# Kernel tuning notes

Measured on AMD Instinct MI355X. Metric: run time of the kernel, lower is better.

Reference implementation:

```python
import jax, jax.numpy as jnp
import numpy as np

B, TQ, TK, D, NA = 8, 512, 2048, 1024, 512
H, HD = 16, 64          # n_head, head_dim (D = H*HD)
NE, HID = 4, 32         # n_experts, expert hidden_dim
EPS = 1e-6


def _rmsnorm(x, w):
    return x * jax.lax.rsqrt(jnp.mean(x * x, axis=-1, keepdims=True) + EPS) * w


def setup_inputs() -> dict:
    key = jax.random.key(0)
    ks = jax.random.split(key, 20)
    r = lambda i, shp: jax.random.normal(ks[i], shp, dtype=jnp.float32) * 0.02
    return {
        'q': jax.random.normal(ks[0], (B, TQ, D), dtype=jnp.float32),
        'kv': jax.random.normal(ks[1], (B, TK, D), dtype=jnp.float32),
        'qn_w': jnp.ones((D,), jnp.float32),
        'kva_w': jnp.ones((D,), jnp.float32),
        'kvi_w': jnp.ones((D,), jnp.float32),
        'dn_w': jnp.ones((D,), jnp.float32),
        'fn_w': jnp.ones((D,), jnp.float32),
        'Wq': r(2, (D, D)), 'bq': jnp.zeros((D,), jnp.float32),
        'Wk': r(3, (D, D)), 'bk': jnp.zeros((D,), jnp.float32),
        'Wv': r(4, (D, D)), 'bv': jnp.zeros((D,), jnp.float32),
        'Wo': r(5, (D, D)), 'bo': jnp.zeros((D,), jnp.float32),
        'active_bias': r(6, (D,)),
        'inactive_bias': r(7, (D,)),
        'log_temp': jnp.array(0.0, jnp.float32),
        'gate_attn': jnp.array(0.3, jnp.float32),
        'gate_ffn': jnp.array(0.7, jnp.float32),
        'Wr': r(8, (D, NE)), 'br': jnp.zeros((NE,), jnp.float32),
        'W1': r(9, (NE, D, 2 * HID)), 'b1': jnp.zeros((NE, 2 * HID), jnp.float32),
        'W2': r(10, (NE, HID, D)), 'b2': jnp.zeros((NE, D), jnp.float32),
        'kv_mask': jnp.ones((B, TK), bool),
        'n_actives': NA,
    }


def _forward(q, kv, qn_w, kva_w, kvi_w, dn_w, fn_w,
             Wq, bq, Wk, bk, Wv, bv, Wo, bo,
             active_bias, inactive_bias, log_temp, gate_attn, gate_ffn,
             Wr, br, W1, b1, W2, b2, kv_mask, n_actives):
    Na = int(n_actives)
    Tk = kv.shape[1]
    Ni = Tk - Na
    b, tq, d = q.shape

    # split-normed kv, with active/inactive learned biases injected pre-KV-proj
    kv_a = _rmsnorm(kv[:, :Na], kva_w) + active_bias
    kv_i = _rmsnorm(kv[:, Na:], kvi_w) + inactive_bias
    kv_b = jnp.concatenate([kv_a, kv_i], axis=1)

    qn = _rmsnorm(q, qn_w)
    qp = (qn @ Wq + bq).reshape(b, tq, H, HD).transpose(0, 2, 1, 3)  # (B,H,Tq,hd)
    k = (kv_b @ Wk + bk).reshape(b, Tk, H, HD).transpose(0, 2, 1, 3)
    v = (kv_b @ Wv + bv).reshape(b, Tk, H, HD).transpose(0, 2, 1, 3)

    # torch: q *= 1/sqrt(hd), then SDPA(q/temp, ...) applies another 1/sqrt(hd)
    temp = jnp.clip(jnp.exp(log_temp), 0.1, 10.0)
    scale = 1.0 / (HD * temp)

    def attn(kk, vv):
        logits = jnp.einsum('bhqd,bhkd->bhqk', qp, kk) * scale
        return jnp.einsum('bhqk,bhkd->bhqd', jax.nn.softmax(logits, axis=-1), vv)

    out = attn(k[:, :, :Na], v[:, :, :Na]) / np.sqrt(max(Na, 1)) \
        - attn(k[:, :, Na:], v[:, :, Na:]) / np.sqrt(max(Ni, 1))
    out = out.transpose(0, 2, 1, 3).reshape(b, tq, d)
    delta = _rmsnorm(out @ Wo + bo, dn_w)
    q_new = q + jax.nn.sigmoid(gate_attn) * delta

    # dense soft MoE over normed kv, with query-similarity logit bias
    x = _rmsnorm(kv, fn_w)
    logits = x @ Wr + br                                   # (B,Tk,NE)
    q_vec = jnp.mean(q_new, axis=1, keepdims=True)         # (B,1,D)
    sim = jnp.einsum('bqd,btd->bt', q_vec, x)              # (B,Tk)
    probs = jax.nn.softmax(logits + sim[..., None], axis=-1)

    h = jnp.einsum('btd,edh->bteh', x, W1) + b1            # (B,Tk,NE,2*HID)
    xp, g = h[..., :HID], h[..., HID:]
    act = xp * (g * jax.nn.sigmoid(g))                     # SwiGLU
    eo = jnp.einsum('bteh,ehd->bted', act, W2) + b2        # (B,Tk,NE,D)
    moe_out = jnp.einsum('bte,bted->btd', probs, eo)

    kv_new = kv + jax.nn.sigmoid(gate_ffn) * moe_out
    return q_new, kv_new


def reference(q, kv, qn_w, kva_w, kvi_w, dn_w, fn_w,
              Wq, bq, Wk, bk, Wv, bv, Wo, bo,
              active_bias, inactive_bias, log_temp, gate_attn, gate_ffn,
              Wr, br, W1, b1, W2, b2, kv_mask, n_actives):
    return _forward(q, kv, qn_w, kva_w, kvi_w, dn_w, fn_w,
                    Wq, bq, Wk, bk, Wv, bv, Wo, bo,
                    active_bias, inactive_bias, log_temp, gate_attn, gate_ffn,
                    Wr, br, W1, b1, W2, b2, kv_mask, n_actives)
```

## Files before the change

kernel.cpp:

```cpp
#include <hip/hip_runtime.h>
#include <hip/hip_bf16.h>
#include <stdint.h>


#define B_   8
#define TQ_  512
#define TK_  2048
#define D_   1024
#define H_   16
#define HD_  64
#define NE_  4
#define HID_ 32
#define EPSF 1e-6f
#define LOG2E 1.44269504f

typedef __bf16 bf16_t;
typedef __bf16 bf16x8 __attribute__((ext_vector_type(8)));
typedef __bf16 bf16x4 __attribute__((ext_vector_type(4)));
typedef float  f32x4  __attribute__((ext_vector_type(4)));

typedef __attribute__((address_space(1))) void gvoid_t;
typedef __attribute__((address_space(3))) void lvoid_t;

__device__ __forceinline__ void gld_lds16(const void* g, void* l) {
  __builtin_amdgcn_global_load_lds((gvoid_t*)g, (lvoid_t*)l, 16, 0, 0);
}

__global__ void transpose_conv_kernel(const float* __restrict__ in, bf16_t* __restrict__ out,
                                      int R, int C, int in_bstride,
                                      int out_rstride, int ob_row, int ob_col) {
  __shared__ float tile[32][33];
  const int bz = blockIdx.z;
  const int rb = blockIdx.y * 32, cb = blockIdx.x * 32;
  const int txi = threadIdx.x, tyi = threadIdx.y;
  const float* inp = in + (size_t)bz * in_bstride;
#pragma unroll
  for (int i = 0; i < 32; i += 8) {
    const int r = rb + tyi + i, c = cb + txi;
    if (r < R && c < C) tile[tyi + i][txi] = inp[(size_t)r * C + c];
  }
  __syncthreads();
#pragma unroll
  for (int i = 0; i < 32; i += 8) {
    const int orow = cb + tyi + i;
    const int ocol = rb + txi;
    if (orow < C && ocol < R)
      out[(size_t)(orow + bz * ob_row) * out_rstride + bz * ob_col + ocol] =
          (bf16_t)tile[txi][tyi + i];
  }
}

__device__ __forceinline__ float block_rsum(float v, float* red) {
  v += __shfl_xor(v, 1);  v += __shfl_xor(v, 2);  v += __shfl_xor(v, 4);
  v += __shfl_xor(v, 8);  v += __shfl_xor(v, 16); v += __shfl_xor(v, 32);
  const int tid = threadIdx.x;
  if ((tid & 63) == 0) red[tid >> 6] = v;
  __syncthreads();
  return red[0] + red[1] + red[2] + red[3];
}

__global__ __launch_bounds__(256)
void rms_kv_kernel(const float* __restrict__ kv, const float* __restrict__ kva_w,
                   const float* __restrict__ kvi_w, const float* __restrict__ fn_w,
                   const float* __restrict__ ab, const float* __restrict__ ib,
                   const int* __restrict__ n_act, const float* __restrict__ Wr,
                   const float* __restrict__ br,
                   bf16_t* __restrict__ kvb, bf16_t* __restrict__ xn,
                   float* __restrict__ probs) {
  __shared__ float red[4];
  __shared__ f32x4 pred[4];
  const int row = blockIdx.x;
  const int t = row & (TK_ - 1);
  const int tid = threadIdx.x;
  const float* src = kv + (size_t)row * D_;
  f32x4 v = ((const f32x4*)src)[tid];
  float ss = v[0]*v[0] + v[1]*v[1] + v[2]*v[2] + v[3]*v[3];
  ss = block_rsum(ss, red);
  const float rs = rsqrtf(ss * (1.0f / D_) + EPSF);
  const int Na = n_act[0];
  const float* wsel = (t < Na) ? kva_w : kvi_w;
  const float* bsel = (t < Na) ? ab : ib;
  const int d = tid * 4;
  f32x4 wv = *(const f32x4*)(wsel + d);
  f32x4 bv = *(const f32x4*)(bsel + d);
  f32x4 fv = *(const f32x4*)(fn_w + d);
  bf16x4 o0, o1;
  f32x4 p4 = {};
#pragma unroll
  for (int c = 0; c < 4; ++c) {
    const float xv = v[c] * rs;
    const float xf = xv * fv[c];
    o0[c] = (bf16_t)(xv * wv[c] + bv[c]);
    o1[c] = (bf16_t)xf;
    const f32x4 w4 = *(const f32x4*)&Wr[(d + c) * 4];
    p4 += w4 * xf;
  }
  *(bf16x4*)&kvb[(size_t)row * D_ + d] = o0;
  *(bf16x4*)&xn [(size_t)row * D_ + d] = o1;
#pragma unroll
  for (int m = 1; m <= 32; m <<= 1) {
    p4[0] += __shfl_xor(p4[0], m); p4[1] += __shfl_xor(p4[1], m);
    p4[2] += __shfl_xor(p4[2], m); p4[3] += __shfl_xor(p4[3], m);
  }
  if ((tid & 63) == 0) pred[tid >> 6] = p4;
  __syncthreads();
  if (tid == 0) {
    f32x4 s = pred[0] + pred[1] + pred[2] + pred[3];
    s[0] += br[0]; s[1] += br[1]; s[2] += br[2]; s[3] += br[3];
    const float mx = fmaxf(fmaxf(s[0], s[1]), fmaxf(s[2], s[3]));
    const float e0 = __expf(s[0] - mx), e1 = __expf(s[1] - mx);
    const float e2 = __expf(s[2] - mx), e3 = __expf(s[3] - mx);
    const float inv = 1.0f / (e0 + e1 + e2 + e3);
    f32x4 pr = { e0 * inv, e1 * inv, e2 * inv, e3 * inv };
    *(f32x4*)&probs[row * 4] = pr;
  }
}

__global__ __launch_bounds__(256)
void rms_q_kernel(const float* __restrict__ q, const float* __restrict__ qn_w,
                  bf16_t* __restrict__ qn) {
  __shared__ float red[4];
  const int row = blockIdx.x;
  const int tid = threadIdx.x;
  const float* src = q + (size_t)row * D_;
  f32x4 v = ((const f32x4*)src)[tid];
  float ss = v[0]*v[0] + v[1]*v[1] + v[2]*v[2] + v[3]*v[3];
  ss = block_rsum(ss, red);
  const float rs = rsqrtf(ss * (1.0f / D_) + EPSF);
  const int d = tid * 4;
  f32x4 wv = *(const f32x4*)(qn_w + d);
  bf16x4 o0;
#pragma unroll
  for (int c = 0; c < 4; ++c) o0[c] = (bf16_t)(v[c] * rs * wv[c]);
  *(bf16x4*)&qn[(size_t)row * D_ + d] = o0;
}

__device__ __forceinline__ void gemm_loop_db(const bf16_t* __restrict__ ga,
                                             const bf16_t* __restrict__ gb,
                                             bf16_t* As, bf16_t* Bs, int K,
                                             size_t rstep, int ar, int br2,
                                             int tid, f32x4 acc[4][4]) {
  gld_lds16(ga,         &As[tid * 8]);
  gld_lds16(ga + rstep, &As[2048 + tid * 8]);
  gld_lds16(gb,         &Bs[tid * 8]);
  gld_lds16(gb + rstep, &Bs[2048 + tid * 8]);
  int buf = 0;
  for (int k0 = 0; k0 < K; k0 += 32) {
    __syncthreads();
    if (k0 + 32 < K) {
      const int nb = buf ^ 1;
      gld_lds16(ga + k0 + 32,         &As[nb * 4096 + tid * 8]);
      gld_lds16(ga + k0 + 32 + rstep, &As[nb * 4096 + 2048 + tid * 8]);
      gld_lds16(gb + k0 + 32,         &Bs[nb * 4096 + tid * 8]);
      gld_lds16(gb + k0 + 32 + rstep, &Bs[nb * 4096 + 2048 + tid * 8]);
    }
    bf16x8 af[4], bfr[4];
#pragma unroll
    for (int i = 0; i < 4; ++i) af[i]  = *(const bf16x8*)&As[buf * 4096 + ar  + i * 512];
#pragma unroll
    for (int j = 0; j < 4; ++j) bfr[j] = *(const bf16x8*)&Bs[buf * 4096 + br2 + j * 512];
#pragma unroll
    for (int i = 0; i < 4; ++i)
#pragma unroll
      for (int j = 0; j < 4; ++j)
        acc[i][j] = __builtin_amdgcn_mfma_f32_16x16x32_bf16(af[i], bfr[j], acc[i][j], 0, 0, 0);
    buf ^= 1;
  }
}

__device__ __forceinline__ int xcd_swz(int bx, int gx) {
  if ((gx & 7) == 0) { const int cpx = gx >> 3; return (bx & 7) * cpx + (bx >> 3); }
  return bx;
}

template<int HAS_BIAS>
__global__ __launch_bounds__(256)
void gemm_tn(const bf16_t* __restrict__ A, const bf16_t* __restrict__ Wt,
             const float* __restrict__ bias, bf16_t* __restrict__ C,
             int M, int N, int K) {
  __shared__ alignas(16) bf16_t As[2 * 128 * 32];
  __shared__ alignas(16) bf16_t Bs[2 * 128 * 32];
  const int tid = threadIdx.x;
  const int lane = tid & 63;
  const int w = tid >> 6;
  const int wr = w >> 1, wc = w & 1;
  const int m0 = xcd_swz(blockIdx.x, gridDim.x) * 128;
  const int n0 = blockIdx.y * 128;

  f32x4 acc[4][4] = {};
  const int eidx = tid * 8;
  const int srow = eidx >> 5;
  const int scol = eidx & 31;
  const bf16_t* ga = A  + (size_t)(m0 + srow) * K + scol;
  const bf16_t* gb = Wt + (size_t)(n0 + srow) * K + scol;
  const int kb = (lane >> 4) * 8;
  const int ar  = (wr * 64 + (lane & 15)) * 32 + kb;
  const int br2 = (wc * 64 + (lane & 15)) * 32 + kb;

  gemm_loop_db(ga, gb, As, Bs, K, (size_t)64 * K, ar, br2, tid, acc);

  const int row0 = m0 + wr * 64 + ((lane >> 4) << 2);
  const int col0 = n0 + wc * 64 + (lane & 15);
#pragma unroll
  for (int j = 0; j < 4; ++j) {
    const int cc = col0 + j * 16;
    const float bv = HAS_BIAS ? bias[cc] : 0.0f;
#pragma unroll
    for (int i = 0; i < 4; ++i) {
      const int rr = row0 + i * 16;
#pragma unroll
      for (int r = 0; r < 4; ++r)
        C[(size_t)(rr + r) * N + cc] = (bf16_t)(acc[i][j][r] + bv);
    }
  }
}

__global__ __launch_bounds__(256)
void gemm_vt(const bf16_t* __restrict__ A, const bf16_t* __restrict__ Wt0,
             const float* __restrict__ bias, bf16_t* __restrict__ C0) {
  __shared__ alignas(16) bf16_t As[2 * 128 * 32];
  __shared__ alignas(16) bf16_t Bs[2 * 128 * 32];
  const int K = D_, N = TK_;
  const bf16_t* Wt = Wt0 + (size_t)blockIdx.z * TK_ * D_;
  bf16_t* C = C0 + (size_t)blockIdx.z * D_ * TK_;
  const int tid = threadIdx.x;
  const int lane = tid & 63;
  const int w = tid >> 6;
  const int wr = w >> 1, wc = w & 1;
  const int m0 = blockIdx.x * 128;
  const int n0 = blockIdx.y * 128;

  f32x4 acc[4][4] = {};
  const int eidx = tid * 8;
  const int srow = eidx >> 5;
  const int scol = eidx & 31;
  const bf16_t* ga = A  + (size_t)(m0 + srow) * K + scol;
  const bf16_t* gb = Wt + (size_t)(n0 + srow) * K + scol;
  const int kb = (lane >> 4) * 8;
  const int ar  = (wr * 64 + (lane & 15)) * 32 + kb;
  const int br2 = (wc * 64 + (lane & 15)) * 32 + kb;

  gemm_loop_db(ga, gb, As, Bs, K, (size_t)64 * K, ar, br2, tid, acc);

  const int row0 = m0 + wr * 64 + ((lane >> 4) << 2);
  const int col0 = n0 + wc * 64 + (lane & 15);
#pragma unroll
  for (int i = 0; i < 4; ++i) {
    const int rr = row0 + i * 16;
#pragma unroll
    for (int r = 0; r < 4; ++r) {
      const float bv = bias[rr + r];
#pragma unroll
      for (int j = 0; j < 4; ++j)
        C[(size_t)(rr + r) * N + col0 + j * 16] = (bf16_t)(acc[i][j][r] + bv);
    }
  }
}

__global__ __launch_bounds__(256)
void gemm_h_act(const bf16_t* __restrict__ A, const bf16_t* __restrict__ Wt,
                const float* __restrict__ bias, const float* __restrict__ probs,
                bf16_t* __restrict__ a2) {
  __shared__ alignas(16) bf16_t As[2 * 128 * 32];
  __shared__ alignas(16) bf16_t Bs[2 * 128 * 32];
  const int K = D_;
  const int tid = threadIdx.x;
  const int lane = tid & 63;
  const int w = tid >> 6;
  const int wr = w >> 1, wc = w & 1;
  const int m0 = xcd_swz(blockIdx.x, gridDim.x) * 128;
  const int n0 = blockIdx.y * 128;

  f32x4 acc[4][4] = {};
  const int eidx = tid * 8;
  const int srow = eidx >> 5;
  const int scol = eidx & 31;
  const bf16_t* ga = A  + (size_t)(m0 + srow) * K + scol;
  const bf16_t* gb = Wt + (size_t)(n0 + srow) * K + scol;
  const int kb = (lane >> 4) * 8;
  const int ar  = (wr * 64 + (lane & 15)) * 32 + kb;
  const int br2 = (wc * 64 + (lane & 15)) * 32 + kb;

  gemm_loop_db(ga, gb, As, Bs, K, (size_t)64 * K, ar, br2, tid, acc);

  const int row0 = m0 + wr * 64 + ((lane >> 4) << 2);
  const int hbase = n0 + wc * 64 + (lane & 15);
  const int e = hbase >> 6;
#pragma unroll
  for (int j = 0; j < 2; ++j) {
    const int ch = hbase + j * 16;
    const float bx = bias[ch], bg = bias[ch + 32];
    const int ac = (ch & 63) + e * 32;
#pragma unroll
    for (int i = 0; i < 4; ++i) {
      const int rr = row0 + i * 16;
#pragma unroll
      for (int r = 0; r < 4; ++r) {
        const float xp = acc[i][j][r] + bx;
        const float g  = acc[i][j + 2][r] + bg;
        const float sg = 1.0f / (1.0f + __expf(-g));
        const float pr = probs[(size_t)(rr + r) * 4 + e];
        a2[(size_t)(rr + r) * 128 + ac] = (bf16_t)(pr * xp * g * sg);
      }
    }
  }
}

__global__ __launch_bounds__(256)
void gemm_moe_kvnew(const bf16_t* __restrict__ A, const bf16_t* __restrict__ Wt,
                    const float* __restrict__ kv, const float* __restrict__ probs,
                    const float* __restrict__ b2, const float* __restrict__ gate_ffn,
                    float* __restrict__ out) {
  __shared__ alignas(16) bf16_t As[2 * 128 * 32];
  __shared__ alignas(16) bf16_t Bs[2 * 128 * 32];
  const int K = 128, N = D_;
  const int tid = threadIdx.x;
  const int lane = tid & 63;
  const int w = tid >> 6;
  const int wr = w >> 1, wc = w & 1;
  const int m0 = xcd_swz(blockIdx.x, gridDim.x) * 128;
  const int n0 = blockIdx.y * 128;

  f32x4 acc[4][4] = {};
  const int eidx = tid * 8;
  const int srow = eidx >> 5;
  const int scol = eidx & 31;
  const bf16_t* ga = A  + (size_t)(m0 + srow) * K + scol;
  const bf16_t* gb = Wt + (size_t)(n0 + srow) * K + scol;
  const int kb = (lane >> 4) * 8;
  const int ar  = (wr * 64 + (lane & 15)) * 32 + kb;
  const int br2 = (wc * 64 + (lane & 15)) * 32 + kb;

  gemm_loop_db(ga, gb, As, Bs, K, (size_t)64 * K, ar, br2, tid, acc);

  const float sgf = 1.0f / (1.0f + __expf(-gate_ffn[0]));
  const int row0 = m0 + wr * 64 + ((lane >> 4) << 2);
  const int col0 = n0 + wc * 64 + (lane & 15);
#pragma unroll
  for (int j = 0; j < 4; ++j) {
    const int cc = col0 + j * 16;
    const f32x4 b2v = { b2[0 * D_ + cc], b2[1 * D_ + cc], b2[2 * D_ + cc], b2[3 * D_ + cc] };
#pragma unroll
    for (int i = 0; i < 4; ++i) {
      const int rr = row0 + i * 16;
#pragma unroll
      for (int r = 0; r < 4; ++r) {
        const f32x4 pr = *(const f32x4*)&probs[(size_t)(rr + r) * 4];
        const float bsum = pr[0]*b2v[0] + pr[1]*b2v[1] + pr[2]*b2v[2] + pr[3]*b2v[3];
        out[(size_t)(rr + r) * N + cc] =
            kv[(size_t)(rr + r) * N + cc] + sgf * (acc[i][j][r] + bsum);
      }
    }
  }
}

__global__ __launch_bounds__(512, 2)
void attn_mfma_kernel(const bf16_t* __restrict__ qp, const bf16_t* __restrict__ kb,
                      const bf16_t* __restrict__ vt, bf16_t* __restrict__ attno,
                      const float* __restrict__ log_temp, const int* __restrict__ n_act) {
  __shared__ alignas(16) bf16_t Ks[2][64 * 64];
  __shared__ alignas(16) bf16_t Vs[2][64 * 64];
  __shared__ alignas(16) bf16_t Ps[8][16 * 64];

  const int dd = blockIdx.x;
  const int xcd = dd & 7, within = dd >> 3;
  const int qt = within & 3, slot0 = within >> 2;
  const int bh = slot0 * 8 + xcd;
  const int b = bh >> 4, h = bh & 15;

  const int tid = threadIdx.x;
  const int lane = tid & 63;
  const int w = tid >> 6;
  const int lane15 = lane & 15, lgrp = lane >> 4, l7 = lane & 7;
  const int Na = n_act[0];
  float temp = __expf(log_temp[0]);
  temp = fminf(fmaxf(temp, 0.1f), 10.0f);
  const float lsc = LOG2E / (64.0f * temp);
  const int q0 = qt * 128;

  const bf16_t* qsrc = qp + (size_t)(b * TQ_ + q0 + w * 16 + lane15) * D_ + h * 64 + lgrp * 8;
  bf16x8 qf0 = *(const bf16x8*)qsrc;
  bf16x8 qf1 = *(const bf16x8*)(qsrc + 32);
#pragma unroll
  for (int j = 0; j < 8; ++j) {
    qf0[j] = (bf16_t)((float)qf0[j] * lsc);
    qf1[j] = (bf16_t)((float)qf1[j] * lsc);
  }

  const int srow = tid >> 3;
  const int schunk = (tid & 7) ^ (srow & 7);
  const bf16_t* ksrc = kb + (size_t)(b * TK_ + srow) * D_ + h * 64 + schunk * 8;
  const bf16_t* vsrc = vt + ((size_t)(b * 16 + h) * 64 + srow) * TK_ + schunk * 8;

  f32x4 o[4] = {};
  f32x4 outa[4] = {};
  float lacc = 0.f;

  const float inv_sa = rsqrtf((float)(Na > 1 ? Na : 1));
  const int Ni = TK_ - Na;
  const float inv_si = rsqrtf((float)(Ni > 1 ? Ni : 1));

  gld_lds16(ksrc, &Ks[0][tid * 8]);
  gld_lds16(vsrc, &Vs[0][tid * 8]);

  for (int t = 0; t < TK_ / 64; ++t) {
    const int cur = t & 1;
    __syncthreads();
    if (t + 1 < TK_ / 64) {
      const int nb = cur ^ 1;
      gld_lds16(ksrc + (size_t)(t + 1) * 64 * D_, &Ks[nb][tid * 8]);
      gld_lds16(vsrc + (size_t)(t + 1) * 64,      &Vs[nb][tid * 8]);
    }

    f32x4 sacc[4];
#pragma unroll
    for (int cf = 0; cf < 4; ++cf) {
      const int krow = (cf * 16 + lane15) * 64;
      const bf16x8 kf0 = *(const bf16x8*)&Ks[cur][krow + ((lgrp ^ l7) << 3)];
      const bf16x8 kf1 = *(const bf16x8*)&Ks[cur][krow + (((lgrp + 4) ^ l7) << 3)];
      f32x4 s = {};
      s = __builtin_amdgcn_mfma_f32_16x16x32_bf16(kf0, qf0, s, 0, 0, 0);
      s = __builtin_amdgcn_mfma_f32_16x16x32_bf16(kf1, qf1, s, 0, 0, 0);
      sacc[cf] = s;
    }

#pragma unroll
    for (int cf = 0; cf < 4; ++cf) {
      f32x4 p;
#pragma unroll
      for (int r = 0; r < 4; ++r) p[r] = exp2f(sacc[cf][r]);
      lacc += (p[0] + p[1]) + (p[2] + p[3]);
      bf16x4 pv4;
#pragma unroll
      for (int r = 0; r < 4; ++r) pv4[r] = (bf16_t)p[r];
      const int c = cf * 2 + (lgrp >> 1);
      *(bf16x4*)&Ps[w][lane15 * 64 + ((c ^ l7) << 3) + (lgrp & 1) * 4] = pv4;
    }

    {
      const int prow = lane15 * 64;
      const bf16x8 pa0 = *(const bf16x8*)&Ps[w][prow + ((lgrp ^ l7) << 3)];
      const bf16x8 pa1 = *(const bf16x8*)&Ps[w][prow + (((lgrp + 4) ^ l7) << 3)];
#pragma unroll
      for (int df = 0; df < 4; ++df) {
        const int vrow = (df * 16 + lane15) * 64;
        const bf16x8 vf0 = *(const bf16x8*)&Vs[cur][vrow + ((lgrp ^ l7) << 3)];
        const bf16x8 vf1 = *(const bf16x8*)&Vs[cur][vrow + (((lgrp + 4) ^ l7) << 3)];
        o[df] = __builtin_amdgcn_mfma_f32_16x16x32_bf16(pa0, vf0, o[df], 0, 0, 0);
        o[df] = __builtin_amdgcn_mfma_f32_16x16x32_bf16(pa1, vf1, o[df], 0, 0, 0);
      }
    }

    const bool endA = ((t + 1) * 64 == Na);
    const bool endI = (t == TK_ / 64 - 1);
    if (endA || endI) {
      float l = lacc;
      l += __shfl_xor(l, 16);
      l += __shfl_xor(l, 32);
      const float ssc = endA ? inv_sa : -inv_si;
      f32x4 iv;
#pragma unroll
      for (int r = 0; r < 4; ++r) iv[r] = ssc / __shfl(l, lgrp * 4 + r);
#pragma unroll
      for (int df = 0; df < 4; ++df) { outa[df] += o[df] * iv; o[df] = (f32x4){}; }
      lacc = 0.f;
    }
  }

#pragma unroll
  for (int df = 0; df < 4; ++df)
#pragma unroll
    for (int r = 0; r < 4; ++r)
      attno[(size_t)(b * TQ_ + q0 + w * 16 + lgrp * 4 + r) * D_ + h * 64 + df * 16 + lane15] =
          (bf16_t)outa[df][r];
}

__global__ __launch_bounds__(256)
void delta_qnew_kernel(const bf16_t* __restrict__ proj, const float* __restrict__ dn_w,
                       const float* __restrict__ q, const float* __restrict__ gate_attn,
                       float* __restrict__ qnew) {
  __shared__ float red[4];
  const int row = blockIdx.x;
  const int tid = threadIdx.x;
  bf16x4 pv = *(const bf16x4*)(proj + (size_t)row * D_ + tid * 4);
  f32x4 v;
#pragma unroll
  for (int c = 0; c < 4; ++c) v[c] = (float)pv[c];
  float ss = v[0]*v[0] + v[1]*v[1] + v[2]*v[2] + v[3]*v[3];
  ss = block_rsum(ss, red);
  const float rs = rsqrtf(ss * (1.0f / D_) + EPSF);
  const float sga = 1.0f / (1.0f + __expf(-gate_attn[0]));
  const int d = tid * 4;
  f32x4 wv = *(const f32x4*)(dn_w + d);
  f32x4 qv = *(const f32x4*)(q + (size_t)row * D_ + d);
  f32x4 out;
#pragma unroll
  for (int c = 0; c < 4; ++c) out[c] = qv[c] + sga * (v[c] * rs * wv[c]);
  *(f32x4*)&qnew[(size_t)row * D_ + d] = out;
}

extern "C" void kernel_launch(void* const* d_in, const int* in_sizes, int n_in,
                              void* d_out, int out_size, void* d_ws, size_t ws_size,
                              hipStream_t stream) {
  const float* q           = (const float*)d_in[0];
  const float* kv          = (const float*)d_in[1];
  const float* qn_w        = (const float*)d_in[2];
  const float* kva_w       = (const float*)d_in[3];
  const float* kvi_w       = (const float*)d_in[4];
  const float* dn_w        = (const float*)d_in[5];
  const float* fn_w        = (const float*)d_in[6];
  const float* Wq          = (const float*)d_in[7];
  const float* bq          = (const float*)d_in[8];
  const float* Wk          = (const float*)d_in[9];
  const float* bk          = (const float*)d_in[10];
  const float* Wv          = (const float*)d_in[11];
  const float* bv          = (const float*)d_in[12];
  const float* Wo          = (const float*)d_in[13];
  const float* bo          = (const float*)d_in[14];
  const float* active_bias = (const float*)d_in[15];
  const float* inactive_b  = (const float*)d_in[16];
  const float* log_temp    = (const float*)d_in[17];
  const float* gate_attn   = (const float*)d_in[18];
  const float* gate_ffn    = (const float*)d_in[19];
  const float* Wr          = (const float*)d_in[20];
  const float* br          = (const float*)d_in[21];
  const float* W1          = (const float*)d_in[22];
  const float* b1          = (const float*)d_in[23];
  const float* W2          = (const float*)d_in[24];
  const float* b2          = (const float*)d_in[25];
  const int*   n_act       = (const int*)d_in[27];

  char* ws = (char*)d_ws;
  size_t off = 0;
  auto alloc = [&](size_t bytes) -> char* {
    char* p = ws + off;
    off = (off + bytes + 255) & ~(size_t)255;
    return p;
  };

  bf16_t* wqT  = (bf16_t*)alloc((size_t)D_ * D_ * 2);
  bf16_t* wkT  = (bf16_t*)alloc((size_t)D_ * D_ * 2);
  bf16_t* wvT  = (bf16_t*)alloc((size_t)D_ * D_ * 2);
  bf16_t* woT  = (bf16_t*)alloc((size_t)D_ * D_ * 2);
  bf16_t* w1T  = (bf16_t*)alloc((size_t)256 * D_ * 2);
  bf16_t* w2T  = (bf16_t*)alloc((size_t)D_ * 128 * 2);
  bf16_t* kvb  = (bf16_t*)alloc((size_t)B_ * TK_ * D_ * 2);
  bf16_t* xn   = (bf16_t*)alloc((size_t)B_ * TK_ * D_ * 2);
  bf16_t* qn   = (bf16_t*)alloc((size_t)B_ * TQ_ * D_ * 2);
  bf16_t* qp   = (bf16_t*)alloc((size_t)B_ * TQ_ * D_ * 2);
  bf16_t* kbuf = (bf16_t*)alloc((size_t)B_ * TK_ * D_ * 2);
  bf16_t* vt   = (bf16_t*)alloc((size_t)B_ * D_ * TK_ * 2);
  float*  probs = (float*)alloc((size_t)B_ * TK_ * NE_ * 4);
  bf16_t* attno = qn;
  bf16_t* proj  = qp;
  bf16_t* a2buf = kbuf;
  (void)ws_size; (void)in_sizes; (void)n_in; (void)out_size;

  float* q_new_out  = (float*)d_out;
  float* kv_new_out = (float*)d_out + (size_t)B_ * TQ_ * D_;

  dim3 tb(32, 8);
  transpose_conv_kernel<<<dim3(32, 32, 1), tb, 0, stream>>>(Wq, wqT, D_, D_, 0, D_, 0, 0);
  transpose_conv_kernel<<<dim3(32, 32, 1), tb, 0, stream>>>(Wk, wkT, D_, D_, 0, D_, 0, 0);
  transpose_conv_kernel<<<dim3(32, 32, 1), tb, 0, stream>>>(Wv, wvT, D_, D_, 0, D_, 0, 0);
  transpose_conv_kernel<<<dim3(32, 32, 1), tb, 0, stream>>>(Wo, woT, D_, D_, 0, D_, 0, 0);
  transpose_conv_kernel<<<dim3(2, 32, 4), tb, 0, stream>>>(W1, w1T, D_, 64, D_ * 64, D_, 64, 0);
  transpose_conv_kernel<<<dim3(32, 1, 4), tb, 0, stream>>>(W2, w2T, 32, D_, 32 * D_, 128, 0, 32);

  rms_kv_kernel<<<B_ * TK_, 256, 0, stream>>>(kv, kva_w, kvi_w, fn_w, active_bias,
                                              inactive_b, n_act, Wr, br, kvb, xn, probs);
  rms_q_kernel<<<B_ * TQ_, 256, 0, stream>>>(q, qn_w, qn);

  gemm_tn<1><<<dim3(B_ * TQ_ / 128, D_ / 128), 256, 0, stream>>>(qn, wqT, bq, qp, B_ * TQ_, D_, D_);
  gemm_tn<1><<<dim3(B_ * TK_ / 128, D_ / 128), 256, 0, stream>>>(kvb, wkT, bk, kbuf, B_ * TK_, D_, D_);
  gemm_vt<<<dim3(D_ / 128, TK_ / 128, B_), 256, 0, stream>>>(wvT, kvb, bv, vt);

  attn_mfma_kernel<<<B_ * H_ * (TQ_ / 128), 512, 0, stream>>>(qp, kbuf, vt, attno, log_temp, n_act);

  gemm_tn<1><<<dim3(B_ * TQ_ / 128, D_ / 128), 256, 0, stream>>>(attno, woT, bo, proj, B_ * TQ_, D_, D_);
  delta_qnew_kernel<<<B_ * TQ_, 256, 0, stream>>>(proj, dn_w, q, gate_attn, q_new_out);

  gemm_h_act<<<dim3(B_ * TK_ / 128, 2), 256, 0, stream>>>(xn, w1T, b1, probs, a2buf);
  gemm_moe_kvnew<<<dim3(B_ * TK_ / 128, D_ / 128), 256, 0, stream>>>(a2buf, w2T, kv, probs, b2,
                                                                     gate_ffn, kv_new_out);
}
```

Measured before the change: 357.3 us.

## Restructure attention to 32 rows per wave, add 64-row GEMMs, batch transposes

The attention kernel drops from 512 to 256 threads per block. Each wave now handles 32 query rows, so every K/V fragment read from LDS feeds two MFMA streams, and s_setprio hints are added around the MFMA sections. New 64-row-tile GEMM variants replace the Q-projection, output-projection and MoE-hidden GEMMs to raise block counts on the smaller problems. The four weight transposes are merged into one launch. In exchange the attention kernel uses more registers per wave and runs with fewer waves per block.

```diff
diff --git a/kernel.cpp b/kernel.cpp
--- a/kernel.cpp
+++ b/kernel.cpp
@@ -24,6 +24,24 @@
 
 __device__ __forceinline__ void gld_lds16(const void* g, void* l) {
   __builtin_amdgcn_global_load_lds((gvoid_t*)g, (lvoid_t*)l, 16, 0, 0);
+}
+
+struct TP4 { const float* in[4]; bf16_t* out[4]; };
+
+__global__ void transpose_conv4_kernel(TP4 p) {
+  __shared__ float tile[32][33];
+  const int bz = blockIdx.z;
+  const float* in = p.in[bz];
+  bf16_t* out = p.out[bz];
+  const int rb = blockIdx.y * 32, cb = blockIdx.x * 32;
+  const int txi = threadIdx.x, tyi = threadIdx.y;
+#pragma unroll
+  for (int i = 0; i < 32; i += 8)
+    tile[tyi + i][txi] = in[(size_t)(rb + tyi + i) * D_ + cb + txi];
+  __syncthreads();
+#pragma unroll
+  for (int i = 0; i < 32; i += 8)
+    out[(size_t)(cb + tyi + i) * D_ + rb + txi] = (bf16_t)tile[txi][tyi + i];
 }
 
 __global__ void transpose_conv_kernel(const float* __restrict__ in, bf16_t* __restrict__ out,
@@ -133,6 +151,11 @@
 #pragma unroll
   for (int c = 0; c < 4; ++c) o0[c] = (bf16_t)(v[c] * rs * wv[c]);
   *(bf16x4*)&qn[(size_t)row * D_ + d] = o0;
+}
+
+__device__ __forceinline__ int xcd_swz(int bx, int gx) {
+  if ((gx & 7) == 0) { const int cpx = gx >> 3; return (bx & 7) * cpx + (bx >> 3); }
+  return bx;
 }
 
 __device__ __forceinline__ void gemm_loop_db(const bf16_t* __restrict__ ga,
@@ -168,9 +191,35 @@
   }
 }
 
-__device__ __forceinline__ int xcd_swz(int bx, int gx) {
-  if ((gx & 7) == 0) { const int cpx = gx >> 3; return (bx & 7) * cpx + (bx >> 3); }
-  return bx;
+__device__ __forceinline__ void gemm64_loop_db(const bf16_t* __restrict__ ga,
+                                               const bf16_t* __restrict__ gb,
+                                               bf16_t* As, bf16_t* Bs, int K,
+                                               size_t rstep, int ar, int br2,
+                                               int tid, f32x4 acc[2][4]) {
+  gld_lds16(ga,         &As[tid * 8]);
+  gld_lds16(gb,         &Bs[tid * 8]);
+  gld_lds16(gb + rstep, &Bs[2048 + tid * 8]);
+  int buf = 0;
+  for (int k0 = 0; k0 < K; k0 += 32) {
+    __syncthreads();
+    if (k0 + 32 < K) {
+      const int nb = buf ^ 1;
+      gld_lds16(ga + k0 + 32,         &As[nb * 2048 + tid * 8]);
+      gld_lds16(gb + k0 + 32,         &Bs[nb * 4096 + tid * 8]);
+      gld_lds16(gb + k0 + 32 + rstep, &Bs[nb * 4096 + 2048 + tid * 8]);
+    }
+    bf16x8 af[2], bfr[4];
+#pragma unroll
+    for (int i = 0; i < 2; ++i) af[i]  = *(const bf16x8*)&As[buf * 2048 + ar  + i * 512];
+#pragma unroll
+    for (int j = 0; j < 4; ++j) bfr[j] = *(const bf16x8*)&Bs[buf * 4096 + br2 + j * 512];
+#pragma unroll
+    for (int i = 0; i < 2; ++i)
+#pragma unroll
+      for (int j = 0; j < 4; ++j)
+        acc[i][j] = __builtin_amdgcn_mfma_f32_16x16x32_bf16(af[i], bfr[j], acc[i][j], 0, 0, 0);
+    buf ^= 1;
+  }
 }
 
 template<int HAS_BIAS>
@@ -188,14 +237,11 @@
   const int n0 = blockIdx.y * 128;
 
   f32x4 acc[4][4] = {};
-  const int eidx = tid * 8;
-  const int srow = eidx >> 5;
-  const int scol = eidx & 31;
-  const bf16_t* ga = A  + (size_t)(m0 + srow) * K + scol;
-  const bf16_t* gb = Wt + (size_t)(n0 + srow) * K + scol;
+  const bf16_t* ga = A  + (size_t)(m0 + (tid >> 2)) * K + (tid & 3) * 8;
+  const bf16_t* gb = Wt + (size_t)(n0 + (tid >> 2)) * K + (tid & 3) * 8;
   const int kb = (lane >> 4) * 8;
-  const int ar  = (wr * 64 + (lane & 15)) * 32 + kb;
-  const int br2 = (wc * 64 + (lane & 15)) * 32 + kb;
+  const int ar  = ((wr * 64 + (lane & 15)) << 5) + kb;
+  const int br2 = ((wc * 64 + (lane & 15)) << 5) + kb;
 
   gemm_loop_db(ga, gb, As, Bs, K, (size_t)64 * K, ar, br2, tid, acc);
 
@@ -207,6 +253,45 @@
     const float bv = HAS_BIAS ? bias[cc] : 0.0f;
 #pragma unroll
     for (int i = 0; i < 4; ++i) {
+      const int rr = row0 + i * 16;
+#pragma unroll
+      for (int r = 0; r < 4; ++r)
+        C[(size_t)(rr + r) * N + cc] = (bf16_t)(acc[i][j][r] + bv);
+    }
+  }
+}
+
+template<int HAS_BIAS>
+__global__ __launch_bounds__(256)
+void gemm64_tn(const bf16_t* __restrict__ A, const bf16_t* __restrict__ Wt,
+               const float* __restrict__ bias, bf16_t* __restrict__ C,
+               int M, int N, int K) {
+  __shared__ alignas(16) bf16_t As[2 * 64 * 32];
+  __shared__ alignas(16) bf16_t Bs[2 * 128 * 32];
+  const int tid = threadIdx.x;
+  const int lane = tid & 63;
+  const int w = tid >> 6;
+  const int wr = w >> 1, wc = w & 1;
+  const int m0 = xcd_swz(blockIdx.x, gridDim.x) * 64;
+  const int n0 = blockIdx.y * 128;
+
+  f32x4 acc[2][4] = {};
+  const bf16_t* ga = A  + (size_t)(m0 + (tid >> 2)) * K + (tid & 3) * 8;
+  const bf16_t* gb = Wt + (size_t)(n0 + (tid >> 2)) * K + (tid & 3) * 8;
+  const int kb = (lane >> 4) * 8;
+  const int ar  = ((wr * 32 + (lane & 15)) << 5) + kb;
+  const int br2 = ((wc * 64 + (lane & 15)) << 5) + kb;
+
+  gemm64_loop_db(ga, gb, As, Bs, K, (size_t)64 * K, ar, br2, tid, acc);
+
+  const int row0 = m0 + wr * 32 + ((lane >> 4) << 2);
+  const int col0 = n0 + wc * 64 + (lane & 15);
+#pragma unroll
+  for (int j = 0; j < 4; ++j) {
+    const int cc = col0 + j * 16;
+    const float bv = HAS_BIAS ? bias[cc] : 0.0f;
+#pragma unroll
+    for (int i = 0; i < 2; ++i) {
       const int rr = row0 + i * 16;
 #pragma unroll
       for (int r = 0; r < 4; ++r)
@@ -231,14 +316,11 @@
   const int n0 = blockIdx.y * 128;
 
   f32x4 acc[4][4] = {};
-  const int eidx = tid * 8;
-  const int srow = eidx >> 5;
-  const int scol = eidx & 31;
-  const bf16_t* ga = A  + (size_t)(m0 + srow) * K + scol;
-  const bf16_t* gb = Wt + (size_t)(n0 + srow) * K + scol;
+  const bf16_t* ga = A  + (size_t)(m0 + (tid >> 2)) * K + (tid & 3) * 8;
+  const bf16_t* gb = Wt + (size_t)(n0 + (tid >> 2)) * K + (tid & 3) * 8;
   const int kb = (lane >> 4) * 8;
-  const int ar  = (wr * 64 + (lane & 15)) * 32 + kb;
-  const int br2 = (wc * 64 + (lane & 15)) * 32 + kb;
+  const int ar  = ((wr * 64 + (lane & 15)) << 5) + kb;
+  const int br2 = ((wc * 64 + (lane & 15)) << 5) + kb;
 
   gemm_loop_db(ga, gb, As, Bs, K, (size_t)64 * K, ar, br2, tid, acc);
 
@@ -258,32 +340,29 @@
 }
 
 __global__ __launch_bounds__(256)
-void gemm_h_act(const bf16_t* __restrict__ A, const bf16_t* __restrict__ Wt,
-                const float* __restrict__ bias, const float* __restrict__ probs,
-                bf16_t* __restrict__ a2) {
-  __shared__ alignas(16) bf16_t As[2 * 128 * 32];
+void gemm64_h_act(const bf16_t* __restrict__ A, const bf16_t* __restrict__ Wt,
+                  const float* __restrict__ bias, const float* __restrict__ probs,
+                  bf16_t* __restrict__ a2) {
+  __shared__ alignas(16) bf16_t As[2 * 64 * 32];
   __shared__ alignas(16) bf16_t Bs[2 * 128 * 32];
   const int K = D_;
   const int tid = threadIdx.x;
   const int lane = tid & 63;
   const int w = tid >> 6;
   const int wr = w >> 1, wc = w & 1;
-  const int m0 = xcd_swz(blockIdx.x, gridDim.x) * 128;
+  const int m0 = xcd_swz(blockIdx.x, gridDim.x) * 64;
   const int n0 = blockIdx.y * 128;
 
-  f32x4 acc[4][4] = {};
-  const int eidx = tid * 8;
-  const int srow = eidx >> 5;
-  const int scol = eidx & 31;
-  const bf16_t* ga = A  + (size_t)(m0 + srow) * K + scol;
-  const bf16_t* gb = Wt + (size_t)(n0 + srow) * K + scol;
+  f32x4 acc[2][4] = {};
+  const bf16_t* ga = A  + (size_t)(m0 + (tid >> 2)) * K + (tid & 3) * 8;
+  const bf16_t* gb = Wt + (size_t)(n0 + (tid >> 2)) * K + (tid & 3) * 8;
   const int kb = (lane >> 4) * 8;
-  const int ar  = (wr * 64 + (lane & 15)) * 32 + kb;
-  const int br2 = (wc * 64 + (lane & 15)) * 32 + kb;
-
-  gemm_loop_db(ga, gb, As, Bs, K, (size_t)64 * K, ar, br2, tid, acc);
-
-  const int row0 = m0 + wr * 64 + ((lane >> 4) << 2);
+  const int ar  = ((wr * 32 + (lane & 15)) << 5) + kb;
+  const int br2 = ((wc * 64 + (lane & 15)) << 5) + kb;
+
+  gemm64_loop_db(ga, gb, As, Bs, K, (size_t)64 * K, ar, br2, tid, acc);
+
+  const int row0 = m0 + wr * 32 + ((lane >> 4) << 2);
   const int hbase = n0 + wc * 64 + (lane & 15);
   const int e = hbase >> 6;
 #pragma unroll
@@ -292,7 +371,7 @@
     const float bx = bias[ch], bg = bias[ch + 32];
     const int ac = (ch & 63) + e * 32;
 #pragma unroll
-    for (int i = 0; i < 4; ++i) {
+    for (int i = 0; i < 2; ++i) {
       const int rr = row0 + i * 16;
 #pragma unroll
       for (int r = 0; r < 4; ++r) {
@@ -322,14 +401,11 @@
   const int n0 = blockIdx.y * 128;
 
   f32x4 acc[4][4] = {};
-  const int eidx = tid * 8;
-  const int srow = eidx >> 5;
-  const int scol = eidx & 31;
-  const bf16_t* ga = A  + (size_t)(m0 + srow) * K + scol;
-  const bf16_t* gb = Wt + (size_t)(n0 + srow) * K + scol;
+  const bf16_t* ga = A  + (size_t)(m0 + (tid >> 2)) * K + (tid & 3) * 8;
+  const bf16_t* gb = Wt + (size_t)(n0 + (tid >> 2)) * K + (tid & 3) * 8;
   const int kb = (lane >> 4) * 8;
-  const int ar  = (wr * 64 + (lane & 15)) * 32 + kb;
-  const int br2 = (wc * 64 + (lane & 15)) * 32 + kb;
+  const int ar  = ((wr * 64 + (lane & 15)) << 5) + kb;
+  const int br2 = ((wc * 64 + (lane & 15)) << 5) + kb;
 
   gemm_loop_db(ga, gb, As, Bs, K, (size_t)64 * K, ar, br2, tid, acc);
 
@@ -354,13 +430,13 @@
   }
 }
 
-__global__ __launch_bounds__(512, 2)
+__global__ __launch_bounds__(256, 3)
 void attn_mfma_kernel(const bf16_t* __restrict__ qp, const bf16_t* __restrict__ kb,
                       const bf16_t* __restrict__ vt, bf16_t* __restrict__ attno,
                       const float* __restrict__ log_temp, const int* __restrict__ n_act) {
   __shared__ alignas(16) bf16_t Ks[2][64 * 64];
   __shared__ alignas(16) bf16_t Vs[2][64 * 64];
-  __shared__ alignas(16) bf16_t Ps[8][16 * 64];
+  __shared__ alignas(16) bf16_t Ps[4][32 * 64];
 
   const int dd = blockIdx.x;
   const int xcd = dd & 7, within = dd >> 3;
@@ -376,15 +452,20 @@
   float temp = __expf(log_temp[0]);
   temp = fminf(fmaxf(temp, 0.1f), 10.0f);
   const float lsc = LOG2E / (64.0f * temp);
-  const int q0 = qt * 128;
-
-  const bf16_t* qsrc = qp + (size_t)(b * TQ_ + q0 + w * 16 + lane15) * D_ + h * 64 + lgrp * 8;
-  bf16x8 qf0 = *(const bf16x8*)qsrc;
-  bf16x8 qf1 = *(const bf16x8*)(qsrc + 32);
+  const int rowbase = qt * 128 + w * 32;
+
+  const bf16_t* qsrcA = qp + (size_t)(b * TQ_ + rowbase + lane15) * D_ + h * 64 + lgrp * 8;
+  const bf16_t* qsrcB = qsrcA + (size_t)16 * D_;
+  bf16x8 qfA0 = *(const bf16x8*)qsrcA;
+  bf16x8 qfA1 = *(const bf16x8*)(qsrcA + 32);
+  bf16x8 qfB0 = *(const bf16x8*)qsrcB;
+  bf16x8 qfB1 = *(const bf16x8*)(qsrcB + 32);
 #pragma unroll
   for (int j = 0; j < 8; ++j) {
-    qf0[j] = (bf16_t)((float)qf0[j] * lsc);
-    qf1[j] = (bf16_t)((float)qf1[j] * lsc);
+    qfA0[j] = (bf16_t)((float)qfA0[j] * lsc);
+    qfA1[j] = (bf16_t)((float)qfA1[j] * lsc);
+    qfB0[j] = (bf16_t)((float)qfB0[j] * lsc);
+    qfB1[j] = (bf16_t)((float)qfB1[j] * lsc);
   }
 
   const int srow = tid >> 3;
@@ -392,87 +473,118 @@
   const bf16_t* ksrc = kb + (size_t)(b * TK_ + srow) * D_ + h * 64 + schunk * 8;
   const bf16_t* vsrc = vt + ((size_t)(b * 16 + h) * 64 + srow) * TK_ + schunk * 8;
 
-  f32x4 o[4] = {};
-  f32x4 outa[4] = {};
-  float lacc = 0.f;
+  f32x4 oA[4] = {}, oB[4] = {}, outA[4] = {}, outB[4] = {};
+  float laccA = 0.f, laccB = 0.f;
 
   const float inv_sa = rsqrtf((float)(Na > 1 ? Na : 1));
   const int Ni = TK_ - Na;
   const float inv_si = rsqrtf((float)(Ni > 1 ? Ni : 1));
 
-  gld_lds16(ksrc, &Ks[0][tid * 8]);
-  gld_lds16(vsrc, &Vs[0][tid * 8]);
+  gld_lds16(ksrc,            &Ks[0][tid * 8]);
+  gld_lds16(ksrc + 32 * D_,  &Ks[0][2048 + tid * 8]);
+  gld_lds16(vsrc,            &Vs[0][tid * 8]);
+  gld_lds16(vsrc + 32 * TK_, &Vs[0][2048 + tid * 8]);
 
   for (int t = 0; t < TK_ / 64; ++t) {
     const int cur = t & 1;
     __syncthreads();
     if (t + 1 < TK_ / 64) {
       const int nb = cur ^ 1;
-      gld_lds16(ksrc + (size_t)(t + 1) * 64 * D_, &Ks[nb][tid * 8]);
-      gld_lds16(vsrc + (size_t)(t + 1) * 64,      &Vs[nb][tid * 8]);
-    }
-
-    f32x4 sacc[4];
+      const bf16_t* kN = ksrc + (size_t)(t + 1) * 64 * D_;
+      const bf16_t* vN = vsrc + (size_t)(t + 1) * 64;
+      gld_lds16(kN,            &Ks[nb][tid * 8]);
+      gld_lds16(kN + 32 * D_,  &Ks[nb][2048 + tid * 8]);
+      gld_lds16(vN,            &Vs[nb][tid * 8]);
+      gld_lds16(vN + 32 * TK_, &Vs[nb][2048 + tid * 8]);
+    }
+
+    f32x4 sA[4], sB[4];
+    __builtin_amdgcn_s_setprio(1);
 #pragma unroll
     for (int cf = 0; cf < 4; ++cf) {
       const int krow = (cf * 16 + lane15) * 64;
       const bf16x8 kf0 = *(const bf16x8*)&Ks[cur][krow + ((lgrp ^ l7) << 3)];
       const bf16x8 kf1 = *(const bf16x8*)&Ks[cur][krow + (((lgrp + 4) ^ l7) << 3)];
       f32x4 s = {};
-      s = __builtin_amdgcn_mfma_f32_16x16x32_bf16(kf0, qf0, s, 0, 0, 0);
-      s = __builtin_amdgcn_mfma_f32_16x16x32_bf16(kf1, qf1, s, 0, 0, 0);
-      sacc[cf] = s;
-    }
+      s = __builtin_amdgcn_mfma_f32_16x16x32_bf16(kf0, qfA0, s, 0, 0, 0);
+      s = __builtin_amdgcn_mfma_f32_16x16x32_bf16(kf1, qfA1, s, 0, 0, 0);
+      sA[cf] = s;
+      f32x4 s2 = {};
+      s2 = __builtin_amdgcn_mfma_f32_16x16x32_bf16(kf0, qfB0, s2, 0, 0, 0);
+      s2 = __builtin_amdgcn_mfma_f32_16x16x32_bf16(kf1, qfB1, s2, 0, 0, 0);
+      sB[cf] = s2;
+    }
+    __builtin_amdgcn_s_setprio(0);
 
 #pragma unroll
     for (int cf = 0; cf < 4; ++cf) {
-      f32x4 p;
-#pragma unroll
-      for (int r = 0; r < 4; ++r) p[r] = exp2f(sacc[cf][r]);
-      lacc += (p[0] + p[1]) + (p[2] + p[3]);
-      bf16x4 pv4;
-#pragma unroll
-      for (int r = 0; r < 4; ++r) pv4[r] = (bf16_t)p[r];
       const int c = cf * 2 + (lgrp >> 1);
-      *(bf16x4*)&Ps[w][lane15 * 64 + ((c ^ l7) << 3) + (lgrp & 1) * 4] = pv4;
+      const int pcol = ((c ^ l7) << 3) + (lgrp & 1) * 4;
+      f32x4 pA, pB;
+#pragma unroll
+      for (int r = 0; r < 4; ++r) pA[r] = exp2f(sA[cf][r]);
+#pragma unroll
+      for (int r = 0; r < 4; ++r) pB[r] = exp2f(sB[cf][r]);
+      laccA += (pA[0] + pA[1]) + (pA[2] + pA[3]);
+      laccB += (pB[0] + pB[1]) + (pB[2] + pB[3]);
+      bf16x4 pvA, pvB;
+#pragma unroll
+      for (int r = 0; r < 4; ++r) { pvA[r] = (bf16_t)pA[r]; pvB[r] = (bf16_t)pB[r]; }
+      *(bf16x4*)&Ps[w][lane15 * 64 + pcol]        = pvA;
+      *(bf16x4*)&Ps[w][(16 + lane15) * 64 + pcol] = pvB;
     }
 
     {
-      const int prow = lane15 * 64;
-      const bf16x8 pa0 = *(const bf16x8*)&Ps[w][prow + ((lgrp ^ l7) << 3)];
-      const bf16x8 pa1 = *(const bf16x8*)&Ps[w][prow + (((lgrp + 4) ^ l7) << 3)];
+      const int prowA = lane15 * 64;
+      const int prowB = (16 + lane15) * 64;
+      const bf16x8 paA0 = *(const bf16x8*)&Ps[w][prowA + ((lgrp ^ l7) << 3)];
+      const bf16x8 paA1 = *(const bf16x8*)&Ps[w][prowA + (((lgrp + 4) ^ l7) << 3)];
+      const bf16x8 paB0 = *(const bf16x8*)&Ps[w][prowB + ((lgrp ^ l7) << 3)];
+      const bf16x8 paB1 = *(const bf16x8*)&Ps[w][prowB + (((lgrp + 4) ^ l7) << 3)];
+      __builtin_amdgcn_s_setprio(1);
 #pragma unroll
       for (int df = 0; df < 4; ++df) {
         const int vrow = (df * 16 + lane15) * 64;
         const bf16x8 vf0 = *(const bf16x8*)&Vs[cur][vrow + ((lgrp ^ l7) << 3)];
         const bf16x8 vf1 = *(const bf16x8*)&Vs[cur][vrow + (((lgrp + 4) ^ l7) << 3)];
-        o[df] = __builtin_amdgcn_mfma_f32_16x16x32_bf16(pa0, vf0, o[df], 0, 0, 0);
-        o[df] = __builtin_amdgcn_mfma_f32_16x16x32_bf16(pa1, vf1, o[df], 0, 0, 0);
+        oA[df] = __builtin_amdgcn_mfma_f32_16x16x32_bf16(paA0, vf0, oA[df], 0, 0, 0);
+        oA[df] = __builtin_amdgcn_mfma_f32_16x16x32_bf16(paA1, vf1, oA[df], 0, 0, 0);
+        oB[df] = __builtin_amdgcn_mfma_f32_16x16x32_bf16(paB0, vf0, oB[df], 0, 0, 0);
+        oB[df] = __builtin_amdgcn_mfma_f32_16x16x32_bf16(paB1, vf1, oB[df], 0, 0, 0);
       }
+      __builtin_amdgcn_s_setprio(0);
     }
 
     const bool endA = ((t + 1) * 64 == Na);
     const bool endI = (t == TK_ / 64 - 1);
     if (endA || endI) {
-      float l = lacc;
-      l += __shfl_xor(l, 16);
-      l += __shfl_xor(l, 32);
+      float lA = laccA, lB = laccB;
+      lA += __shfl_xor(lA, 16); lA += __shfl_xor(lA, 32);
+      lB += __shfl_xor(lB, 16); lB += __shfl_xor(lB, 32);
       const float ssc = endA ? inv_sa : -inv_si;
-      f32x4 iv;
-#pragma unroll
-      for (int r = 0; r < 4; ++r) iv[r] = ssc / __shfl(l, lgrp * 4 + r);
-#pragma unroll
-      for (int df = 0; df < 4; ++df) { outa[df] += o[df] * iv; o[df] = (f32x4){}; }
-      lacc = 0.f;
+      f32x4 ivA, ivB;
+#pragma unroll
+      for (int r = 0; r < 4; ++r) {
+        ivA[r] = ssc / __shfl(lA, lgrp * 4 + r);
+        ivB[r] = ssc / __shfl(lB, lgrp * 4 + r);
+      }
+#pragma unroll
+      for (int df = 0; df < 4; ++df) {
+        outA[df] += oA[df] * ivA; oA[df] = (f32x4){};
+        outB[df] += oB[df] * ivB; oB[df] = (f32x4){};
+      }
+      laccA = 0.f; laccB = 0.f;
     }
   }
 
 #pragma unroll
   for (int df = 0; df < 4; ++df)
 #pragma unroll
-    for (int r = 0; r < 4; ++r)
-      attno[(size_t)(b * TQ_ + q0 + w * 16 + lgrp * 4 + r) * D_ + h * 64 + df * 16 + lane15] =
-          (bf16_t)outa[df][r];
+    for (int r = 0; r < 4; ++r) {
+      const size_t ro = (size_t)(b * TQ_ + rowbase + lgrp * 4 + r) * D_ + h * 64 + df * 16 + lane15;
+      attno[ro]             = (bf16_t)outA[df][r];
+      attno[ro + 16 * D_]   = (bf16_t)outB[df][r];
+    }
 }
 
 __global__ __launch_bounds__(256)
@@ -560,10 +672,10 @@
   float* kv_new_out = (float*)d_out + (size_t)B_ * TQ_ * D_;
 
   dim3 tb(32, 8);
-  transpose_conv_kernel<<<dim3(32, 32, 1), tb, 0, stream>>>(Wq, wqT, D_, D_, 0, D_, 0, 0);
-  transpose_conv_kernel<<<dim3(32, 32, 1), tb, 0, stream>>>(Wk, wkT, D_, D_, 0, D_, 0, 0);
-  transpose_conv_kernel<<<dim3(32, 32, 1), tb, 0, stream>>>(Wv, wvT, D_, D_, 0, D_, 0, 0);
-  transpose_conv_kernel<<<dim3(32, 32, 1), tb, 0, stream>>>(Wo, woT, D_, D_, 0, D_, 0, 0);
+  TP4 tp;
+  tp.in[0] = Wq; tp.in[1] = Wk; tp.in[2] = Wv; tp.in[3] = Wo;
+  tp.out[0] = wqT; tp.out[1] = wkT; tp.out[2] = wvT; tp.out[3] = woT;
+  transpose_conv4_kernel<<<dim3(32, 32, 4), tb, 0, stream>>>(tp);
   transpose_conv_kernel<<<dim3(2, 32, 4), tb, 0, stream>>>(W1, w1T, D_, 64, D_ * 64, D_, 64, 0);
   transpose_conv_kernel<<<dim3(32, 1, 4), tb, 0, stream>>>(W2, w2T, 32, D_, 32 * D_, 128, 0, 32);
 
@@ -571,16 +683,16 @@
                                               inactive_b, n_act, Wr, br, kvb, xn, probs);
   rms_q_kernel<<<B_ * TQ_, 256, 0, stream>>>(q, qn_w, qn);
 
-  gemm_tn<1><<<dim3(B_ * TQ_ / 128, D_ / 128), 256, 0, stream>>>(qn, wqT, bq, qp, B_ * TQ_, D_, D_);
+  gemm64_tn<1><<<dim3(B_ * TQ_ / 64, D_ / 128), 256, 0, stream>>>(qn, wqT, bq, qp, B_ * TQ_, D_, D_);
   gemm_tn<1><<<dim3(B_ * TK_ / 128, D_ / 128), 256, 0, stream>>>(kvb, wkT, bk, kbuf, B_ * TK_, D_, D_);
   gemm_vt<<<dim3(D_ / 128, TK_ / 128, B_), 256, 0, stream>>>(wvT, kvb, bv, vt);
 
-  attn_mfma_kernel<<<B_ * H_ * (TQ_ / 128), 512, 0, stream>>>(qp, kbuf, vt, attno, log_temp, n_act);
-
-  gemm_tn<1><<<dim3(B_ * TQ_ / 128, D_ / 128), 256, 0, stream>>>(attno, woT, bo, proj, B_ * TQ_, D_, D_);
+  attn_mfma_kernel<<<B_ * H_ * (TQ_ / 128), 256, 0, stream>>>(qp, kbuf, vt, attno, log_temp, n_act);
+
+  gemm64_tn<1><<<dim3(B_ * TQ_ / 64, D_ / 128), 256, 0, stream>>>(attno, woT, bo, proj, B_ * TQ_, D_, D_);
   delta_qnew_kernel<<<B_ * TQ_, 256, 0, stream>>>(proj, dn_w, q, gate_attn, q_new_out);
 
-  gemm_h_act<<<dim3(B_ * TK_ / 128, 2), 256, 0, stream>>>(xn, w1T, b1, probs, a2buf);
+  gemm64_h_act<<<dim3(B_ * TK_ / 64, 2), 256, 0, stream>>>(xn, w1T, b1, probs, a2buf);
   gemm_moe_kvnew<<<dim3(B_ * TK_ / 128, D_ / 128), 256, 0, stream>>>(a2buf, w2T, kv, probs, b2,
                                                                      gate_ffn, kv_new_out);
 }
```

Measured after the change: 339.4 us. 5.0% less time.
